# Kernel optimization log

Measured on AMD Instinct MI355X. Metric: run time of the kernel, lower is better.

Reference implementation:

```python
import jax, jax.numpy as jnp
import numpy as np

D_MODEL = 1024
NUM_HEADS = 16
D_K = D_MODEL // NUM_HEADS
NEG = -1.0e9


def setup_inputs() -> dict:
    key = jax.random.key(0)
    ks = jax.random.split(key, 12)
    B, L = 2, 2048
    s = 1.0 / np.sqrt(D_MODEL)
    inp = {
        "query": jax.random.normal(ks[0], (B, L, D_MODEL), jnp.float32),
        "key": jax.random.normal(ks[1], (B, L, D_MODEL), jnp.float32),
        "value": jax.random.normal(ks[2], (B, L, D_MODEL), jnp.float32),
        "hash_q": jax.random.randint(ks[3], (B, NUM_HEADS, L), 0, 2, jnp.int32),
        "hash_k": jax.random.randint(ks[4], (B, NUM_HEADS, L), 0, 2, jnp.int32),
        # nn.Linear weights stored as [out, in] like torch; applied as x @ W.T + b
        "Wq": jax.random.normal(ks[5], (D_MODEL, D_MODEL), jnp.float32) * s,
        "bq": jnp.zeros((D_MODEL,), jnp.float32),
        "Wk": jax.random.normal(ks[6], (D_MODEL, D_MODEL), jnp.float32) * s,
        "bk": jnp.zeros((D_MODEL,), jnp.float32),
        "Wv": jax.random.normal(ks[7], (D_MODEL, D_MODEL), jnp.float32) * s,
        "bv": jnp.zeros((D_MODEL,), jnp.float32),
    }
    return inp


def _split_heads(x, B, L):
    # [B, L, D] -> [B, H, L, d_k]
    return x.reshape(B, L, NUM_HEADS, D_K).transpose(0, 2, 1, 3)


def reference(query, key, value, hash_q, hash_k, Wq, bq, Wk, bk, Wv, bv):
    B, Lq, _ = query.shape
    Lk = key.shape[1]
    q = _split_heads(query @ Wq.T + bq, B, Lq)   # [B,H,Lq,dk]
    k = _split_heads(key @ Wk.T + bk, B, Lk)     # [B,H,Lk,dk]
    v = _split_heads(value @ Wv.T + bv, B, Lk)   # [B,H,Lk,dk]

    scores = jnp.einsum("bhqd,bhkd->bhqk", q, k) / jnp.sqrt(jnp.float32(D_K))
    mask = (hash_q[:, :, :, None] != hash_k[:, :, None, :]).astype(scores.dtype) * NEG
    attn = jax.nn.softmax(scores + mask, axis=-1)
    out = jnp.einsum("bhqk,bhkd->bhqd", attn, v)  # [B,H,Lq,dk]
    return out.transpose(0, 2, 1, 3).reshape(B, Lq, D_MODEL)
```

## Files before the change

### kernel.cpp

```cpp
#include <hip/hip_runtime.h>
#include <hip/hip_bf16.h>
#include <stdint.h>
#include <math.h>

#define NHEAD 16
#define DK 64
#define SEQ 2048
#define BATCH 2
#define DMODEL 1024

typedef __attribute__((ext_vector_type(8))) short short8_t;
typedef __attribute__((ext_vector_type(4))) short short4_t;
typedef __attribute__((ext_vector_type(4))) float f32x4;

#define MFMA(a, b, c) __builtin_amdgcn_mfma_f32_16x16x32_bf16(a, b, c, 0, 0, 0)
#define MFMA16(a, b, c) __builtin_amdgcn_mfma_f32_16x16x16bf16_1k(a, b, c, 0, 0, 0)

__device__ __forceinline__ unsigned short f2bf(float f) {
    union { __hip_bfloat16 b; unsigned short u; } c;
    c.b = __float2bfloat16(f);
    return c.u;
}

__global__ __launch_bounds__(256) void bucket_cvt_kernel(
    const int* __restrict__ hq, const int* __restrict__ hk,
    int* __restrict__ qorder, int* __restrict__ korder,
    int* __restrict__ qinv, int* __restrict__ kinv, int* __restrict__ cnts,
    const float* __restrict__ X0, const float* __restrict__ X1,
    const float* __restrict__ X2,
    const float* __restrict__ W0, const float* __restrict__ W1,
    const float* __restrict__ W2,
    unsigned short* __restrict__ xo0, unsigned short* __restrict__ xo1,
    unsigned short* __restrict__ xo2,
    unsigned short* __restrict__ wo0, unsigned short* __restrict__ wo1,
    unsigned short* __restrict__ wo2)
{
    __shared__ int cnt[257];
    const int t = threadIdx.x;
    if (blockIdx.x < 64) {
        const int blk = blockIdx.x;
        const int bh = blk >> 1;
        const int which = blk & 1;
        const int* src = (which ? hk : hq) + (size_t)bh * SEQ;
        int* dst = (which ? korder : qorder) + (size_t)bh * SEQ;
        int* ivd = (which ? kinv : qinv) + (size_t)bh * SEQ;

        int h[8]; int c = 0;
#pragma unroll
        for (int j = 0; j < 8; j++) { h[j] = src[t * 8 + j]; c += (h[j] == 0); }
        cnt[t] = c;
        __syncthreads();
        if (t == 0) {
            int run = 0;
            for (int i = 0; i < 256; i++) { int v = cnt[i]; cnt[i] = run; run += v; }
            cnt[256] = run;
        }
        __syncthreads();
        const int nz = cnt[256];
        int zpos = cnt[t];
        int opos = nz + t * 8 - cnt[t];
#pragma unroll
        for (int j = 0; j < 8; j++) {
            int idx = t * 8 + j;
            if (h[j] == 0) { dst[zpos] = idx; ivd[idx] = zpos; zpos++; }
            else           { dst[opos] = idx; ivd[idx] = opos; opos++; }
        }
        if (t == 0) cnts[which * 32 + bh] = nz;
        return;
    }

    const size_t g = (size_t)(blockIdx.x - 64) * 256 + t;
    const float* s; unsigned short* d; size_t off;
    if (g < 1572864) {
        int which = (int)(g / 524288);
        off = (g % 524288) * 8;
        s = which == 0 ? X0 : (which == 1 ? X1 : X2);
        d = which == 0 ? xo0 : (which == 1 ? xo1 : xo2);
    } else {
        size_t g2 = g - 1572864;
        int which = (int)(g2 / 131072);
        off = (g2 % 131072) * 8;
        s = which == 0 ? W0 : (which == 1 ? W1 : W2);
        d = which == 0 ? wo0 : (which == 1 ? wo1 : wo2);
    }
    f32x4 v0 = *(const f32x4*)(s + off);
    f32x4 v1 = *(const f32x4*)(s + off + 4);
    union { short8_t v; unsigned short u[8]; } o;
#pragma unroll
    for (int j = 0; j < 4; j++) {
        o.u[j]     = f2bf(v0[j]);
        o.u[4 + j] = f2bf(v1[j]);
    }
    *(short8_t*)(d + off) = o.v;
}

__global__ __launch_bounds__(256) void bucket_kernel(
    const int* __restrict__ hq, const int* __restrict__ hk,
    int* __restrict__ qorder, int* __restrict__ korder,
    int* __restrict__ qinv, int* __restrict__ kinv, int* __restrict__ cnts)
{
    const int blk = blockIdx.x;
    const int bh = blk >> 1;
    const int which = blk & 1;
    const int* src = (which ? hk : hq) + (size_t)bh * SEQ;
    int* dst = (which ? korder : qorder) + (size_t)bh * SEQ;
    int* ivd = (which ? kinv : qinv) + (size_t)bh * SEQ;

    __shared__ int cnt[257];
    const int t = threadIdx.x;
    int h[8]; int c = 0;
#pragma unroll
    for (int j = 0; j < 8; j++) { h[j] = src[t * 8 + j]; c += (h[j] == 0); }
    cnt[t] = c;
    __syncthreads();
    if (t == 0) {
        int run = 0;
        for (int i = 0; i < 256; i++) { int v = cnt[i]; cnt[i] = run; run += v; }
        cnt[256] = run;
    }
    __syncthreads();
    const int nz = cnt[256];
    int zpos = cnt[t];
    int opos = nz + t * 8 - cnt[t];
#pragma unroll
    for (int j = 0; j < 8; j++) {
        int idx = t * 8 + j;
        if (h[j] == 0) { dst[zpos] = idx; ivd[idx] = zpos; zpos++; }
        else           { dst[opos] = idx; ivd[idx] = opos; opos++; }
    }
    if (t == 0) cnts[which * 32 + bh] = nz;
}

__global__ __launch_bounds__(256) void cvt_xw_kernel(
    const float* __restrict__ X, const float* __restrict__ W,
    unsigned short* __restrict__ Xb, unsigned short* __restrict__ Wb)
{
    const size_t t = (size_t)blockIdx.x * 256 + threadIdx.x;
    const float* src;
    unsigned short* dst;
    size_t i8;
    if (t < 524288) { src = X; dst = Xb; i8 = t * 8; }
    else            { src = W; dst = Wb; i8 = (t - 524288) * 8; }
    f32x4 v0 = *(const f32x4*)(src + i8);
    f32x4 v1 = *(const f32x4*)(src + i8 + 4);
    union { short8_t v; unsigned short u[8]; } o;
#pragma unroll
    for (int j = 0; j < 4; j++) {
        o.u[j]     = f2bf(v0[j]);
        o.u[4 + j] = f2bf(v1[j]);
    }
    *(short8_t*)(dst + i8) = o.v;
}

__global__ __launch_bounds__(256) void proj_kernel(
    const unsigned short* __restrict__ Xq, const unsigned short* __restrict__ Xk,
    const unsigned short* __restrict__ Xv,
    const unsigned short* __restrict__ Wq, const unsigned short* __restrict__ Wk,
    const unsigned short* __restrict__ Wv,
    const float* __restrict__ bq, const float* __restrict__ bk,
    const float* __restrict__ bv,
    const int* __restrict__ qinv, const int* __restrict__ kinv,
    unsigned short* __restrict__ pQ, unsigned short* __restrict__ pK,
    unsigned short* __restrict__ pVn, int grpBase)
{
    __shared__ unsigned short At[2][128 * 64];
    __shared__ unsigned short Bt[2][64 * 64];

    const int tid = threadIdx.x;
    const int lane = tid & 63;
    const int wv = tid >> 6;
    const int fr = lane & 15;
    const int fg = lane >> 4;
    const int srw = lane >> 3;
    const int su = lane & 7;

    const int grp = grpBase + (blockIdx.x >> 9);
    const int local = blockIdx.x & 511;
    const int xg = local & 7;
    const int j = local >> 3;
    const bool mode1 = (grp == 2);

    const unsigned short* Xb = grp == 0 ? Xq : (grp == 1 ? Xk : Xv);
    const unsigned short* Wb = grp == 0 ? Wq : (grp == 1 ? Wk : Wv);
    const float* bias = grp == 0 ? bq : (grp == 1 ? bk : bv);
    const int* inv = grp == 0 ? qinv : kinv;
    unsigned short* dst = grp == 0 ? pQ : (grp == 1 ? pK : pVn);

    const unsigned short* Ap; const unsigned short* Bp;
    int m0, n0;
    if (!mode1) {
        Ap = Xb; Bp = Wb;
        m0 = ((xg << 2) + (j >> 4)) * 128;
        n0 = (j & 15) * 64;
    } else {
        Ap = Wb; Bp = Xb;
        m0 = (j & 7) * 128;
        n0 = ((xg << 3) + (j >> 3)) * 64;
    }

    const unsigned short* aS[4]; const unsigned short* bS[2];
#pragma unroll
    for (int i = 0; i < 4; i++) {
        int r = wv * 32 + i * 8 + srw;
        aS[i] = Ap + (size_t)(m0 + r) * DMODEL + ((su ^ (r & 7)) << 3);
    }
#pragma unroll
    for (int i = 0; i < 2; i++) {
        int r = wv * 16 + i * 8 + srw;
        bS[i] = Bp + (size_t)(n0 + r) * DMODEL + ((su ^ (r & 7)) << 3);
    }

    f32x4 acc[2][4];
    const f32x4 fzero = {0.f, 0.f, 0.f, 0.f};
#pragma unroll
    for (int mf = 0; mf < 2; mf++)
#pragma unroll
        for (int nf = 0; nf < 4; nf++) acc[mf][nf] = fzero;

#define PSTAGE(K0, BI)                                                        \
    {                                                                         \
        _Pragma("unroll")                                                     \
        for (int i = 0; i < 4; i++)                                           \
            __builtin_amdgcn_global_load_lds(                                 \
                (const void*)(aS[i] + (K0)),                                  \
                (void*)&At[BI][(wv * 32 + i * 8) * 64], 16, 0, 0);            \
        _Pragma("unroll")                                                     \
        for (int i = 0; i < 2; i++)                                           \
            __builtin_amdgcn_global_load_lds(                                 \
                (const void*)(bS[i] + (K0)),                                  \
                (void*)&Bt[BI][(wv * 16 + i * 8) * 64], 16, 0, 0);            \
    }

    PSTAGE(0, 0);
    int cur = 0;

    for (int kk = 0; kk < 16; kk++) {
        if (kk < 15) {
            PSTAGE((kk + 1) * 64, cur ^ 1);
            asm volatile("s_waitcnt vmcnt(6)" ::: "memory");
        } else {
            asm volatile("s_waitcnt vmcnt(0)" ::: "memory");
        }
        __builtin_amdgcn_sched_barrier(0);
        __builtin_amdgcn_s_barrier();
        __builtin_amdgcn_sched_barrier(0);

        short8_t a[2][2], b[4][2];
#pragma unroll
        for (int mf = 0; mf < 2; mf++)
#pragma unroll
            for (int ks = 0; ks < 2; ks++) {
                int r = wv * 32 + mf * 16 + fr;
                int u = (ks * 4 + fg) ^ (fr & 7);
                a[mf][ks] = *(const short8_t*)&At[cur][r * 64 + u * 8];
            }
#pragma unroll
        for (int nf = 0; nf < 4; nf++)
#pragma unroll
            for (int ks = 0; ks < 2; ks++) {
                int r = nf * 16 + fr;
                int u = (ks * 4 + fg) ^ (fr & 7);
                b[nf][ks] = *(const short8_t*)&Bt[cur][r * 64 + u * 8];
            }
#pragma unroll
        for (int ks = 0; ks < 2; ks++)
#pragma unroll
            for (int mf = 0; mf < 2; mf++)
#pragma unroll
                for (int nf = 0; nf < 4; nf++)
                    acc[mf][nf] = MFMA(a[mf][ks], b[nf][ks], acc[mf][nf]);

        __builtin_amdgcn_sched_barrier(0);
        __builtin_amdgcn_s_barrier();
        __builtin_amdgcn_sched_barrier(0);
        cur ^= 1;
    }
#undef PSTAGE

    if (!mode1) {
        const int hh = n0 >> 6;
#pragma unroll
        for (int mf = 0; mf < 2; mf++)
#pragma unroll
            for (int r = 0; r < 4; r++) {
                int gm = m0 + wv * 32 + mf * 16 + fg * 4 + r;
                int bb = gm >> 11;
                int bh = bb * NHEAD + hh;
                int pos = inv[(size_t)bh * SEQ + (gm & (SEQ - 1))];
                unsigned short* drow = dst + ((size_t)bh * SEQ + pos) * DK;
#pragma unroll
                for (int nf = 0; nf < 4; nf++) {
                    float v = acc[mf][nf][r] + bias[n0 + nf * 16 + fr];
                    drow[nf * 16 + fr] = f2bf(v);
                }
            }
    } else {
        const int bb = n0 >> 11;
#pragma unroll
        for (int mf = 0; mf < 2; mf++)
#pragma unroll
            for (int r = 0; r < 4; r++) {
                int od = m0 + wv * 32 + mf * 16 + fg * 4 + r;
                int h = od >> 6;
                int bh = bb * NHEAD + h;
                float bvv = bias[od];
                unsigned short* drow =
                    dst + ((size_t)bh * DK + (od & 63)) * SEQ + (n0 & (SEQ - 1));
#pragma unroll
                for (int nf = 0; nf < 4; nf++) {
                    float v = acc[mf][nf][r] + bvv;
                    drow[nf * 16 + fr] = f2bf(v);
                }
            }
    }
}

__global__ __launch_bounds__(256) void vperm_kernel(
    const unsigned short* __restrict__ Vn, const int* __restrict__ korder,
    unsigned short* __restrict__ Vs)
{
    const int blk = blockIdx.x;
    const int bh = blk >> 6;
    const int d  = blk & 63;
    const int t = threadIdx.x;
    const int* kop = korder + (size_t)bh * SEQ + t * 8;
    const unsigned short* src = Vn + ((size_t)bh * DK + d) * SEQ;
    union { short8_t v; unsigned short u[8]; } o;
#pragma unroll
    for (int j = 0; j < 8; j++) o.u[j] = src[kop[j]];
    *(short8_t*)(Vs + ((size_t)bh * DK + d) * SEQ + t * 8) = o.v;
}

__global__ __launch_bounds__(256, 4) void lsh_attn_kernel(
    const unsigned short* __restrict__ Qs,
    const unsigned short* __restrict__ Ks, const unsigned short* __restrict__ Vst,
    const int* __restrict__ qorder, const int* __restrict__ cnts,
    float* __restrict__ out)
{
    __shared__ unsigned short KtL[2][64 * 64];
    __shared__ unsigned short VtL[2][64 * 64];

    const int tid = threadIdx.x;
    const int lane = tid & 63;
    const int wv = tid >> 6;
    const int fr = lane & 15;
    const int fg = lane >> 4;

    const int flat = blockIdx.x;
    const int xcd = flat & 7;
    const int s2 = flat >> 3;
    const int bh = (xcd << 2) + (s2 / 33);
    const int slot = s2 % 33;

    const int nq0 = cnts[bh];
    const int nk0 = cnts[32 + bh];
    const int c0 = (nq0 + 63) >> 6;

    int B, qlo, qhi;
    if (slot < c0) {
        B = 0; qlo = slot << 6; qhi = min(qlo + 64, nq0);
    } else {
        B = 1; qlo = nq0 + ((slot - c0) << 6);
        if (qlo >= SEQ) return;
        qhi = min(qlo + 64, SEQ);
    }
    const int klo = B ? (nk0 >> 6) : 0;
    const int khi = B ? (SEQ >> 6) : ((nk0 + 63) >> 6);
    const int nt = khi - klo;

    const size_t base = (size_t)bh * SEQ * DK;
    const unsigned short* Kb = Ks + base;
    const unsigned short* Vb = Vst + (size_t)bh * DK * SEQ;

    const int srw = lane >> 3;
    const int su = lane & 7;

    short8_t q_hi[2];
    {
        const size_t ro = base + (size_t)(qlo + wv * 16 + fr) * DK;
        q_hi[0] = *(const short8_t*)(Qs + ro + fg * 8);
        q_hi[1] = *(const short8_t*)(Qs + ro + 32 + fg * 8);
    }

    const int swz = fr & 7;
    const int u0 = ((fg ^ swz) << 3);
    const int u1 = (((4 + fg) ^ swz) << 3);
    int vuoff[4];
#pragma unroll
    for (int kg = 0; kg < 4; kg++)
        vuoff[kg] = (((kg * 2 + (fg >> 1)) ^ swz) << 3) + ((fg & 1) << 2);

    const float C2 = 0.18033688011112042f;
    const float B2 = -14.426950408889634f;

    const short4_t ones = {(short)0x3F80, (short)0x3F80, (short)0x3F80, (short)0x3F80};
    f32x4 acc_sum;
    f32x4 o_acc[4];
    const f32x4 fzero = {0.f, 0.f, 0.f, 0.f};
    acc_sum = fzero;
#pragma unroll
    for (int t = 0; t < 4; t++) o_acc[t] = fzero;

#define STAGE(T, BI)                                                          \
    {                                                                         \
        const int k0s = (T) << 6;                                             \
        _Pragma("unroll")                                                     \
        for (int i = 0; i < 2; i++) {                                         \
            const int r = wv * 16 + i * 8 + srw;                              \
            const int uo = ((su ^ (r & 7)) << 3);                             \
            __builtin_amdgcn_global_load_lds(                                 \
                (const void*)(Kb + (size_t)(k0s + r) * DK + uo),              \
                (void*)&KtL[BI][(wv * 16 + i * 8) * 64], 16, 0, 0);           \
            __builtin_amdgcn_global_load_lds(                                 \
                (const void*)(Vb + (size_t)r * SEQ + k0s + uo),               \
                (void*)&VtL[BI][(wv * 16 + i * 8) * 64], 16, 0, 0);           \
        }                                                                     \
    }

    STAGE(klo, 0);
    int cur = 0;

    for (int i = 0; i < nt; i++) {
        if (i + 1 < nt) {
            STAGE(klo + i + 1, cur ^ 1);
            asm volatile("s_waitcnt vmcnt(4)" ::: "memory");
        } else {
            asm volatile("s_waitcnt vmcnt(0)" ::: "memory");
        }
        __builtin_amdgcn_sched_barrier(0);
        __builtin_amdgcn_s_barrier();
        __builtin_amdgcn_sched_barrier(0);

        const int k0 = (klo + i) << 6;

        short4_t vfr[4][4];
#pragma unroll
        for (int dt = 0; dt < 4; dt++)
#pragma unroll
            for (int kg = 0; kg < 4; kg++)
                vfr[dt][kg] = *(const short4_t*)&VtL[cur][(dt * 16 + fr) * 64 + vuoff[kg]];

        f32x4 s[4];
#pragma unroll
        for (int kg = 0; kg < 4; kg++) {
            const int rr = (kg * 16 + fr) * 64;
            short8_t kc0 = *(const short8_t*)&KtL[cur][rr + u0];
            short8_t kc1 = *(const short8_t*)&KtL[cur][rr + u1];
            f32x4 a = fzero;
            a = MFMA(kc0, q_hi[0], a);
            a = MFMA(kc1, q_hi[1], a);
            s[kg] = a;
        }

        short4_t pk[4];
        const bool mixed = B ? (k0 < nk0) : (k0 + 64 > nk0);
        if (!mixed) {
#pragma unroll
            for (int kg = 0; kg < 4; kg++) {
                union { short4_t v; unsigned short u[4]; } P;
#pragma unroll
                for (int r = 0; r < 4; r++)
                    P.u[r] = f2bf(exp2f(fmaf(s[kg][r], C2, B2)));
                pk[kg] = P.v;
            }
        } else {
#pragma unroll
            for (int kg = 0; kg < 4; kg++) {
                union { short4_t v; unsigned short u[4]; } P;
#pragma unroll
                for (int r = 0; r < 4; r++) {
                    int cb = (k0 + kg * 16 + fg * 4 + r) >= nk0;
                    float basev = (cb == B) ? B2 : -1e9f;
                    P.u[r] = f2bf(exp2f(fmaf(s[kg][r], C2, basev)));
                }
                pk[kg] = P.v;
            }
        }

#pragma unroll
        for (int kg = 0; kg < 4; kg++)
            acc_sum = MFMA16(ones, pk[kg], acc_sum);

#pragma unroll
        for (int dt = 0; dt < 4; dt++) {
            f32x4 acc = o_acc[dt];
#pragma unroll
            for (int kg = 0; kg < 4; kg++)
                acc = MFMA16(vfr[dt][kg], pk[kg], acc);
            o_acc[dt] = acc;
        }

        __builtin_amdgcn_sched_barrier(0);
        __builtin_amdgcn_s_barrier();
        __builtin_amdgcn_sched_barrier(0);
        cur ^= 1;
    }
#undef STAGE

    const float psum = acc_sum[0];

    const int b = bh >> 4, h = bh & 15;
    const int qpos = qlo + wv * 16 + fr;
    if (qpos < qhi) {
        const int origq = qorder[(size_t)bh * SEQ + qpos];
        const float inv = 1.0f / psum;
        float* orow = out + ((size_t)(b * SEQ + origq)) * DMODEL + h * DK + fg * 4;
#pragma unroll
        for (int dt = 0; dt < 4; dt++) {
            f32x4 v = o_acc[dt];
            v *= inv;
            *(f32x4*)(orow + dt * 16) = v;
        }
    }
}


extern "C" void kernel_launch(void* const* d_in, const int* in_sizes, int n_in,
                              void* d_out, int out_size, void* d_ws, size_t ws_size,
                              hipStream_t stream)
{
    const float* query = (const float*)d_in[0];
    const float* key   = (const float*)d_in[1];
    const float* value = (const float*)d_in[2];
    const int* hash_q  = (const int*)d_in[3];
    const int* hash_k  = (const int*)d_in[4];
    const float* Wq    = (const float*)d_in[5];
    const float* bq    = (const float*)d_in[6];
    const float* Wk    = (const float*)d_in[7];
    const float* bk    = (const float*)d_in[8];
    const float* Wv    = (const float*)d_in[9];
    const float* bv    = (const float*)d_in[10];
    float* out = (float*)d_out;

    const size_t plane = (size_t)BATCH * NHEAD * SEQ * DK;
    const size_t wsz = (size_t)DMODEL * DMODEL;

    const size_t needFused =
        (4 * plane + 3 * plane + 3 * wsz) * sizeof(unsigned short) +
        (4 * 65536 + 64) * sizeof(int);

    if (ws_size >= needFused) {
        unsigned short* ws = (unsigned short*)d_ws;
        unsigned short* pQ  = ws;
        unsigned short* pK  = ws + plane;
        unsigned short* pVt = ws + 2 * plane;
        unsigned short* pVn = ws + 3 * plane;
        unsigned short* xq  = ws + 4 * plane;
        unsigned short* xk  = xq + plane;
        unsigned short* xv  = xk + plane;
        unsigned short* wqb = xv + plane;
        unsigned short* wkb = wqb + wsz;
        unsigned short* wvb = wkb + wsz;
        int* ip = (int*)(wvb + wsz);
        int* qorder = ip;
        int* korder = ip + 65536;
        int* qinv   = ip + 131072;
        int* kinv   = ip + 196608;
        int* cnts   = ip + 262144;

        bucket_cvt_kernel<<<64 + 7680, 256, 0, stream>>>(
            hash_q, hash_k, qorder, korder, qinv, kinv, cnts,
            query, key, value, Wq, Wk, Wv,
            xq, xk, xv, wqb, wkb, wvb);

        proj_kernel<<<1536, 256, 0, stream>>>(
            xq, xk, xv, wqb, wkb, wvb, bq, bk, bv,
            qinv, kinv, pQ, pK, pVn, 0);

        vperm_kernel<<<2048, 256, 0, stream>>>(pVn, korder, pVt);

        lsh_attn_kernel<<<dim3(1056), 256, 0, stream>>>(pQ, pK, pVt,
                                                        qorder, cnts, out);
    } else {
        unsigned short* ws = (unsigned short*)d_ws;
        unsigned short* pQ    = ws;
        unsigned short* pK    = ws + plane;
        unsigned short* pVt   = ws + 2 * plane;
        unsigned short* pVn   = ws + 3 * plane;
        unsigned short* Xslot = ws + 4 * plane;
        unsigned short* Wslot = ws + 5 * plane;
        int* ip = (int*)(ws + 5 * plane + wsz);
        int* qorder = ip;
        int* korder = ip + 65536;
        int* qinv   = ip + 131072;
        int* kinv   = ip + 196608;
        int* cnts   = ip + 262144;

        bucket_kernel<<<64, 256, 0, stream>>>(hash_q, hash_k, qorder, korder,
                                              qinv, kinv, cnts);

        const int cvtBlocks = (int)((plane + wsz) / 8 / 256);

        cvt_xw_kernel<<<cvtBlocks, 256, 0, stream>>>(query, Wq, Xslot, Wslot);
        proj_kernel<<<512, 256, 0, stream>>>(Xslot, Xslot, Xslot,
                                             Wslot, Wslot, Wslot, bq, bq, bq,
                                             qinv, qinv, pQ, pQ, pQ, 0);

        cvt_xw_kernel<<<cvtBlocks, 256, 0, stream>>>(key, Wk, Xslot, Wslot);
        proj_kernel<<<512, 256, 0, stream>>>(Xslot, Xslot, Xslot,
                                             Wslot, Wslot, Wslot, bk, bk, bk,
                                             kinv, kinv, pK, pK, pK, 1);

        cvt_xw_kernel<<<cvtBlocks, 256, 0, stream>>>(value, Wv, Xslot, Wslot);
        proj_kernel<<<512, 256, 0, stream>>>(Xslot, Xslot, Xslot,
                                             Wslot, Wslot, Wslot, bv, bv, bv,
                                             kinv, kinv, pVn, pVn, pVn, 2);

        vperm_kernel<<<2048, 256, 0, stream>>>(pVn, korder, pVt);

        lsh_attn_kernel<<<dim3(1056), 256, 0, stream>>>(pQ, pK, pVt,
                                                        qorder, cnts, out);
    }
}
```

Baseline: 105.8 us.

## Enlarge projection GEMM tile to 128x128 and raise MFMA wave priority

The projection GEMM tile grows from 128x64 to 128x128, so each block loads a larger B tile and each wave holds twice as many accumulators. This halves the block count and raises reuse of the A fragments loaded from LDS. The inner loop now interleaves B fragment loads with MFMAs, and s_setprio is added around the MFMA sections of both the projection and attention kernels. The cost is more LDS and registers per block (launch bounds now request 2 blocks per CU) and fewer blocks to fill the GPU. The epilogue is also reworked so each 128-column tile writes into two heads.

```diff
diff --git a/kernel.cpp b/kernel.cpp
--- a/kernel.cpp
+++ b/kernel.cpp
@@ -152,7 +152,7 @@
     *(short8_t*)(dst + i8) = o.v;
 }
 
-__global__ __launch_bounds__(256) void proj_kernel(
+__global__ __launch_bounds__(256, 2) void proj_kernel(
     const unsigned short* __restrict__ Xq, const unsigned short* __restrict__ Xk,
     const unsigned short* __restrict__ Xv,
     const unsigned short* __restrict__ Wq, const unsigned short* __restrict__ Wk,
@@ -164,7 +164,7 @@
     unsigned short* __restrict__ pVn, int grpBase)
 {
     __shared__ unsigned short At[2][128 * 64];
-    __shared__ unsigned short Bt[2][64 * 64];
+    __shared__ unsigned short Bt[2][128 * 64];
 
     const int tid = threadIdx.x;
     const int lane = tid & 63;
@@ -174,8 +174,8 @@
     const int srw = lane >> 3;
     const int su = lane & 7;
 
-    const int grp = grpBase + (blockIdx.x >> 9);
-    const int local = blockIdx.x & 511;
+    const int grp = grpBase + (blockIdx.x >> 8);
+    const int local = blockIdx.x & 255;
     const int xg = local & 7;
     const int j = local >> 3;
     const bool mode1 = (grp == 2);
@@ -190,45 +190,40 @@
     int m0, n0;
     if (!mode1) {
         Ap = Xb; Bp = Wb;
-        m0 = ((xg << 2) + (j >> 4)) * 128;
-        n0 = (j & 15) * 64;
+        m0 = ((xg << 2) + (j & 3)) * 128;
+        n0 = (j >> 2) * 128;
     } else {
         Ap = Wb; Bp = Xb;
-        m0 = (j & 7) * 128;
-        n0 = ((xg << 3) + (j >> 3)) * 64;
-    }
-
-    const unsigned short* aS[4]; const unsigned short* bS[2];
+        m0 = (j >> 2) * 128;
+        n0 = ((xg << 2) + (j & 3)) * 128;
+    }
+
+    const unsigned short* aS[4]; const unsigned short* bS[4];
 #pragma unroll
     for (int i = 0; i < 4; i++) {
         int r = wv * 32 + i * 8 + srw;
         aS[i] = Ap + (size_t)(m0 + r) * DMODEL + ((su ^ (r & 7)) << 3);
-    }
-#pragma unroll
-    for (int i = 0; i < 2; i++) {
-        int r = wv * 16 + i * 8 + srw;
         bS[i] = Bp + (size_t)(n0 + r) * DMODEL + ((su ^ (r & 7)) << 3);
     }
 
-    f32x4 acc[2][4];
+    f32x4 acc[2][8];
     const f32x4 fzero = {0.f, 0.f, 0.f, 0.f};
 #pragma unroll
     for (int mf = 0; mf < 2; mf++)
 #pragma unroll
-        for (int nf = 0; nf < 4; nf++) acc[mf][nf] = fzero;
+        for (int nf = 0; nf < 8; nf++) acc[mf][nf] = fzero;
 
 #define PSTAGE(K0, BI)                                                        \
     {                                                                         \
         _Pragma("unroll")                                                     \
-        for (int i = 0; i < 4; i++)                                           \
+        for (int i = 0; i < 4; i++) {                                         \
             __builtin_amdgcn_global_load_lds(                                 \
                 (const void*)(aS[i] + (K0)),                                  \
                 (void*)&At[BI][(wv * 32 + i * 8) * 64], 16, 0, 0);            \
-        _Pragma("unroll")                                                     \
-        for (int i = 0; i < 2; i++)                                           \
             __builtin_amdgcn_global_load_lds(                                 \
                 (const void*)(bS[i] + (K0)),                                  \
-                (void*)&Bt[BI][(wv * 16 + i * 8) * 64], 16, 0, 0);            \
+                (void*)&Bt[BI][(wv * 32 + i * 8) * 64], 16, 0, 0);            \
+        }                                                                     \
     }
 
     PSTAGE(0, 0);
@@ -237,7 +232,7 @@
     for (int kk = 0; kk < 16; kk++) {
         if (kk < 15) {
             PSTAGE((kk + 1) * 64, cur ^ 1);
-            asm volatile("s_waitcnt vmcnt(6)" ::: "memory");
+            asm volatile("s_waitcnt vmcnt(8)" ::: "memory");
         } else {
             asm volatile("s_waitcnt vmcnt(0)" ::: "memory");
         }
@@ -245,7 +240,7 @@
         __builtin_amdgcn_s_barrier();
         __builtin_amdgcn_sched_barrier(0);
 
-        short8_t a[2][2], b[4][2];
+        short8_t a[2][2];
 #pragma unroll
         for (int mf = 0; mf < 2; mf++)
 #pragma unroll
@@ -254,21 +249,20 @@
                 int u = (ks * 4 + fg) ^ (fr & 7);
                 a[mf][ks] = *(const short8_t*)&At[cur][r * 64 + u * 8];
             }
-#pragma unroll
-        for (int nf = 0; nf < 4; nf++)
-#pragma unroll
-            for (int ks = 0; ks < 2; ks++) {
-                int r = nf * 16 + fr;
-                int u = (ks * 4 + fg) ^ (fr & 7);
-                b[nf][ks] = *(const short8_t*)&Bt[cur][r * 64 + u * 8];
-            }
-#pragma unroll
-        for (int ks = 0; ks < 2; ks++)
-#pragma unroll
-            for (int mf = 0; mf < 2; mf++)
-#pragma unroll
-                for (int nf = 0; nf < 4; nf++)
-                    acc[mf][nf] = MFMA(a[mf][ks], b[nf][ks], acc[mf][nf]);
+        __builtin_amdgcn_s_setprio(1);
+#pragma unroll
+        for (int nf = 0; nf < 8; nf++) {
+            int rB = nf * 16 + fr;
+            int ub0 = (fg ^ (fr & 7)) << 3;
+            int ub1 = ((4 + fg) ^ (fr & 7)) << 3;
+            short8_t b0 = *(const short8_t*)&Bt[cur][rB * 64 + ub0];
+            short8_t b1 = *(const short8_t*)&Bt[cur][rB * 64 + ub1];
+            acc[0][nf] = MFMA(a[0][0], b0, acc[0][nf]);
+            acc[0][nf] = MFMA(a[0][1], b1, acc[0][nf]);
+            acc[1][nf] = MFMA(a[1][0], b0, acc[1][nf]);
+            acc[1][nf] = MFMA(a[1][1], b1, acc[1][nf]);
+        }
+        __builtin_amdgcn_s_setprio(0);
 
         __builtin_amdgcn_sched_barrier(0);
         __builtin_amdgcn_s_barrier();
@@ -278,24 +272,29 @@
 #undef PSTAGE
 
     if (!mode1) {
-        const int hh = n0 >> 6;
 #pragma unroll
         for (int mf = 0; mf < 2; mf++)
 #pragma unroll
             for (int r = 0; r < 4; r++) {
                 int gm = m0 + wv * 32 + mf * 16 + fg * 4 + r;
                 int bb = gm >> 11;
-                int bh = bb * NHEAD + hh;
-                int pos = inv[(size_t)bh * SEQ + (gm & (SEQ - 1))];
-                unsigned short* drow = dst + ((size_t)bh * SEQ + pos) * DK;
-#pragma unroll
-                for (int nf = 0; nf < 4; nf++) {
-                    float v = acc[mf][nf][r] + bias[n0 + nf * 16 + fr];
-                    drow[nf * 16 + fr] = f2bf(v);
+                int ml = gm & (SEQ - 1);
+                int bh0 = bb * NHEAD + (n0 >> 6);
+                int pos0 = inv[(size_t)bh0 * SEQ + ml];
+                int pos1 = inv[(size_t)(bh0 + 1) * SEQ + ml];
+                unsigned short* d0 = dst + ((size_t)bh0 * SEQ + pos0) * DK;
+                unsigned short* d1 = dst + ((size_t)(bh0 + 1) * SEQ + pos1) * DK;
+#pragma unroll
+                for (int nf = 0; nf < 8; nf++) {
+                    int col = nf * 16 + fr;
+                    float v = acc[mf][nf][r] + bias[n0 + col];
+                    if (col < 64) d0[col] = f2bf(v);
+                    else          d1[col - 64] = f2bf(v);
                 }
             }
     } else {
         const int bb = n0 >> 11;
+        const int ml = n0 & (SEQ - 1);
 #pragma unroll
         for (int mf = 0; mf < 2; mf++)
 #pragma unroll
@@ -305,9 +304,9 @@
                 int bh = bb * NHEAD + h;
                 float bvv = bias[od];
                 unsigned short* drow =
-                    dst + ((size_t)bh * DK + (od & 63)) * SEQ + (n0 & (SEQ - 1));
-#pragma unroll
-                for (int nf = 0; nf < 4; nf++) {
+                    dst + ((size_t)bh * DK + (od & 63)) * SEQ + ml;
+#pragma unroll
+                for (int nf = 0; nf < 8; nf++) {
                     float v = acc[mf][nf][r] + bvv;
                     drow[nf * 16 + fr] = f2bf(v);
                 }
@@ -433,6 +432,8 @@
 
         const int k0 = (klo + i) << 6;
 
+        __builtin_amdgcn_s_setprio(1);
+
         short4_t vfr[4][4];
 #pragma unroll
         for (int dt = 0; dt < 4; dt++)
@@ -489,6 +490,8 @@
                 acc = MFMA16(vfr[dt][kg], pk[kg], acc);
             o_acc[dt] = acc;
         }
+
+        __builtin_amdgcn_s_setprio(0);
 
         __builtin_amdgcn_sched_barrier(0);
         __builtin_amdgcn_s_barrier();
@@ -563,7 +566,7 @@
             query, key, value, Wq, Wk, Wv,
             xq, xk, xv, wqb, wkb, wvb);
 
-        proj_kernel<<<1536, 256, 0, stream>>>(
+        proj_kernel<<<768, 256, 0, stream>>>(
             xq, xk, xv, wqb, wkb, wvb, bq, bk, bv,
             qinv, kinv, pQ, pK, pVn, 0);
 
@@ -592,17 +595,17 @@
         const int cvtBlocks = (int)((plane + wsz) / 8 / 256);
 
         cvt_xw_kernel<<<cvtBlocks, 256, 0, stream>>>(query, Wq, Xslot, Wslot);
-        proj_kernel<<<512, 256, 0, stream>>>(Xslot, Xslot, Xslot,
+        proj_kernel<<<256, 256, 0, stream>>>(Xslot, Xslot, Xslot,
                                              Wslot, Wslot, Wslot, bq, bq, bq,
                                              qinv, qinv, pQ, pQ, pQ, 0);
 
         cvt_xw_kernel<<<cvtBlocks, 256, 0, stream>>>(key, Wk, Xslot, Wslot);
-        proj_kernel<<<512, 256, 0, stream>>>(Xslot, Xslot, Xslot,
+        proj_kernel<<<256, 256, 0, stream>>>(Xslot, Xslot, Xslot,
                                              Wslot, Wslot, Wslot, bk, bk, bk,
                                              kinv, kinv, pK, pK, pK, 1);
 
         cvt_xw_kernel<<<cvtBlocks, 256, 0, stream>>>(value, Wv, Xslot, Wslot);
-        proj_kernel<<<512, 256, 0, stream>>>(Xslot, Xslot, Xslot,
+        proj_kernel<<<256, 256, 0, stream>>>(Xslot, Xslot, Xslot,
                                              Wslot, Wslot, Wslot, bv, bv, bv,
                                              kinv, kinv, pVn, pVn, pVn, 2);
 
```

Result: slower. 112.5 us (+6.4%).
